# Optimization experiments

Hardware: AMD Instinct MI355X
Metric: run time of the kernel (lower is better)

Reference implementation:

```python
import jax, jax.numpy as jnp
import numpy as np

B, S, D, H, DK = 2, 2048, 256, 8, 32


def setup_inputs() -> dict:
    key = jax.random.key(0)
    ks = jax.random.split(key, 12)
    inp = {
        "query": jax.random.normal(ks[0], (B, S, D), jnp.float32),
        "key_": jax.random.normal(ks[1], (B, S, D), jnp.float32),
        "value": jax.random.normal(ks[2], (B, S, D), jnp.float32),
        "mask": jax.random.randint(ks[3], (B, S, S), 0, 2).astype(bool),
        "relation": jax.random.normal(ks[4], (B, S, S), jnp.float32) * 0.05,
        # learned params (Linear stores y = x @ W^T; we store W already transposed)
        "Wq": jax.random.normal(ks[5], (D, H * DK), jnp.float32) * 0.02,
        "Wk": jax.random.normal(ks[6], (D, H * DK), jnp.float32) * 0.02,
        "Wv": jax.random.normal(ks[7], (D, H * DK), jnp.float32) * 0.02,
        "Wfc": jax.random.normal(ks[8], (H * DK, D), jnp.float32) * 0.02,
        "bfc": jax.random.normal(ks[9], (D,), jnp.float32) * 0.02,
        "gamma": jnp.ones((D,), jnp.float32),
        "beta": jnp.zeros((D,), jnp.float32),
    }
    return inp


def _layernorm(x, gamma, beta, eps=1e-5):
    mu = jnp.mean(x, axis=-1, keepdims=True)
    var = jnp.var(x, axis=-1, keepdims=True)
    return (x - mu) * jax.lax.rsqrt(var + eps) * gamma + beta


def reference(query, key_, value, mask, relation, Wq, Wk, Wv, Wfc, bfc, gamma, beta):
    b, s, _ = query.shape
    def split_heads(x, W):
        return (x @ W).reshape(b, s, H, DK).transpose(0, 2, 1, 3)  # [B,H,S,DK]
    Q = split_heads(query, Wq)
    K = split_heads(key_, Wk)
    V = split_heads(value, Wv)
    # (Q K^T) @ relation / sqrt(dk)   -- relation broadcast over heads
    qk = jnp.einsum('bhqd,bhkd->bhqk', Q, K)          # [B,H,S,S]
    scores = jnp.einsum('bhqk,bkn->bhqn', qk, relation) / jnp.sqrt(jnp.float32(DK))
    scores = jnp.where(mask[:, None, :, :], jnp.float32(-1e9), scores)
    attn = jax.nn.softmax(scores, axis=-1)            # dropout in eval mode = identity
    att = jnp.einsum('bhqn,bhnd->bhqd', attn, V)      # [B,H,S,DK]
    att = att.transpose(0, 2, 1, 3).reshape(b, s, H * DK)
    out = att @ Wfc + bfc
    return _layernorm(out + query, gamma, beta), attn
```

## Files before the change

### kernel.cpp

```cpp
#include <hip/hip_runtime.h>

constexpr int Bc = 2, Sc = 2048, Dc = 256, Hc = 8, DKc = 32;
constexpr int BH = Bc * Hc;

typedef _Float16 f16x8 __attribute__((ext_vector_type(8)));
typedef _Float16 f16x4 __attribute__((ext_vector_type(4)));
typedef float    f32x4 __attribute__((ext_vector_type(4)));

__global__ __launch_bounds__(256) void prep_kernel(
    const float* __restrict__ query, const float* __restrict__ key_,
    const float* __restrict__ value, const float* __restrict__ Wq,
    const float* __restrict__ Wk, const float* __restrict__ Wv,
    const float* __restrict__ rel, const unsigned int* __restrict__ mask,
    _Float16* __restrict__ Qb, _Float16* __restrict__ Kt,
    _Float16* __restrict__ Vt, _Float16* __restrict__ relT,
    unsigned int* __restrict__ mbits)
{
    __shared__ __align__(16) char smem[16640];
    const int bx = blockIdx.x;
    const int t = threadIdx.x;
    if (bx < 1536) {
        constexpr int ROWS = 8;
        float (*xs)[Dc] = (float(*)[Dc])smem;
        const int z = bx >> 9;
        const int lb = bx & 511;
        const float* X = (z == 0) ? query : (z == 1) ? key_ : value;
        const float* W = (z == 0) ? Wq : (z == 1) ? Wk : Wv;
        _Float16* out = (z == 0) ? Qb : (z == 1) ? Kt : Vt;
        const int vtrans = (z != 0);
        const float scale = (z == 0) ? 0.17677669529663689f : 1.0f;
        const int r0 = lb * ROWS;
        #pragma unroll
        for (int i = 0; i < ROWS; ++i)
            xs[i][t] = X[(long)(r0 + i) * Dc + t];
        __syncthreads();
        float acc[ROWS];
        #pragma unroll
        for (int i = 0; i < ROWS; ++i) acc[i] = 0.f;
        for (int d = 0; d < Dc; ++d) {
            float w = W[d * Dc + t];
            #pragma unroll
            for (int i = 0; i < ROWS; ++i) acc[i] = fmaf(xs[i][d], w, acc[i]);
        }
        const int h = t >> 5, dk = t & 31;
        #pragma unroll
        for (int i = 0; i < ROWS; ++i) {
            int row = r0 + i;
            int b = row >> 11, s = row & 2047;
            long idx = vtrans ? (((long)(b * Hc + h) * DKc + dk) * Sc + s)
                              : (((long)(b * Hc + h) * Sc + s) * DKc + dk);
            out[idx] = (_Float16)(acc[i] * scale);
        }
    } else if (bx < 3584) {
        float (*tile)[65] = (float(*)[65])smem;
        const int idx = bx - 1536;
        const int b = idx >> 10;
        const int rem = idx & 1023;
        const int k0 = (rem >> 5) * 64, n0 = (rem & 31) * 64;
        const int r = t >> 4;
        const int c4 = (t & 15) * 4;
        const float* src = rel + (long)b * Sc * Sc;
        #pragma unroll
        for (int i = 0; i < 4; ++i) {
            f32x4 v = *(const f32x4*)&src[(long)(k0 + i * 16 + r) * Sc + n0 + c4];
            *(f32x4*)&tile[i * 16 + r][c4] = v;
        }
        __syncthreads();
        _Float16* dst = relT + (long)b * Sc * Sc;
        #pragma unroll
        for (int i = 0; i < 4; ++i) {
            const int n = i * 16 + r;
            f16x4 o;
            #pragma unroll
            for (int e = 0; e < 4; ++e) o[e] = (_Float16)tile[c4 + e][n];
            *(f16x4*)&dst[(long)(n0 + n) * Sc + k0 + c4] = o;
        }
    } else {
        const int idx = (bx - 3584) * 256 + t;
        const uint4 a = ((const uint4*)mask)[idx * 2];
        const uint4 b = ((const uint4*)mask)[idx * 2 + 1];
        unsigned int wsv[8] = {a.x, a.y, a.z, a.w, b.x, b.y, b.z, b.w};
        unsigned int r = 0;
        #pragma unroll
        for (int j = 0; j < 8; ++j) {
            unsigned int nib = (wsv[j] | (wsv[j] >> 7) | (wsv[j] >> 14) | (wsv[j] >> 21)) & 0xFu;
            r |= nib << (4 * j);
        }
        mbits[idx] = r;
    }
}

__global__ __launch_bounds__(256) void kr_kernel(
    const _Float16* __restrict__ relT, const _Float16* __restrict__ Kt,
    _Float16* __restrict__ KRT)
{
    constexpr int LDK = 72;
    __shared__ _Float16 As[64][LDK];
    __shared__ _Float16 Bs[64][LDK];
    const int b = blockIdx.z;
    const int m0 = blockIdx.y * 64;
    const int n0 = blockIdx.x * 64;
    const _Float16* Ap = relT + (long)b * Sc * Sc;
    const _Float16* Bp = Kt + (long)b * Hc * DKc * Sc;
    const int t = threadIdx.x;
    const int lane = t & 63, wave = t >> 6;
    const int wr = wave >> 1, wc = wave & 1;
    const int c = lane & 15, g = lane >> 4;
    const int lrow = t >> 2;
    const int lcol = (t & 3) * 16;
    f32x4 acc[2][2] = {};
    for (int k0 = 0; k0 < Sc; k0 += 64) {
        *(f16x8*)&As[lrow][lcol]     = *(const f16x8*)&Ap[(long)(m0 + lrow) * Sc + k0 + lcol];
        *(f16x8*)&As[lrow][lcol + 8] = *(const f16x8*)&Ap[(long)(m0 + lrow) * Sc + k0 + lcol + 8];
        *(f16x8*)&Bs[lrow][lcol]     = *(const f16x8*)&Bp[(long)(n0 + lrow) * Sc + k0 + lcol];
        *(f16x8*)&Bs[lrow][lcol + 8] = *(const f16x8*)&Bp[(long)(n0 + lrow) * Sc + k0 + lcol + 8];
        __syncthreads();
        #pragma unroll
        for (int kk = 0; kk < 2; ++kk) {
            const int kb = kk * 32 + g * 8;
            f16x8 af[2], bf[2];
            #pragma unroll
            for (int m = 0; m < 2; ++m)
                af[m] = *(const f16x8*)&As[wr * 32 + m * 16 + c][kb];
            #pragma unroll
            for (int n = 0; n < 2; ++n)
                bf[n] = *(const f16x8*)&Bs[wc * 32 + n * 16 + c][kb];
            #pragma unroll
            for (int m = 0; m < 2; ++m)
                #pragma unroll
                for (int n = 0; n < 2; ++n)
                    acc[m][n] = __builtin_amdgcn_mfma_f32_16x16x32_f16(
                        af[m], bf[n], acc[m][n], 0, 0, 0);
        }
        __syncthreads();
    }
    _Float16* outp = KRT + (long)b * Sc * 256;
    #pragma unroll
    for (int m = 0; m < 2; ++m)
        #pragma unroll
        for (int n = 0; n < 2; ++n)
            #pragma unroll
            for (int i = 0; i < 4; ++i) {
                int row = m0 + wr * 32 + m * 16 + g * 4 + i;
                int col = n0 + wc * 32 + n * 16 + c;
                outp[(long)row * 256 + col] = (_Float16)acc[m][n][i];
            }
}

__global__ __launch_bounds__(256) void attn_pv_kernel(
    const _Float16* __restrict__ Qb,
    const _Float16* __restrict__ KRT,
    const _Float16* __restrict__ Vt,
    const unsigned int* __restrict__ mbits,
    float* __restrict__ esum_p,
    float* __restrict__ accp)
{
    constexpr int NT = 128, LDP = 136;
    __shared__ _Float16 p_lds[64][LDP];
    const int bh = blockIdx.y;
    const int ns = blockIdx.z;
    const int b = bh >> 3, h = bh & 7;
    const int q0 = blockIdx.x * 64;
    const int t = threadIdx.x, lane = t & 63, w = t >> 6;
    const int c = lane & 15, g = lane >> 4;
    const int q = q0 + w * 16 + c;
    const f16x8 qf = *(const f16x8*)&Qb[((long)bh * Sc + q) * DKc + g * 8];
    const _Float16* krt = KRT + (long)b * Sc * 256 + h * 32;
    const unsigned int* mbitrow = mbits + ((long)b * Sc + q) * (Sc / 32);
    const f32x4 zero = {};
    f32x4 acc[2] = {};
    float esum = 0.f;

    for (int nt = ns * 4; nt < ns * 4 + 4; ++nt) {
        const int n0 = nt * NT;
        f32x4 s[8];
        #pragma unroll
        for (int nf = 0; nf < 8; ++nf) {
            f16x8 kf = *(const f16x8*)&krt[(long)(n0 + nf * 16 + c) * 256 + g * 8];
            s[nf] = __builtin_amdgcn_mfma_f32_16x16x32_f16(kf, qf, zero, 0, 0, 0);
        }
        const uint4 mq = *(const uint4*)&mbitrow[nt * 4];
        const unsigned int mwv[4] = {mq.x, mq.y, mq.z, mq.w};
        #pragma unroll
        for (int nf = 0; nf < 8; ++nf) {
            const unsigned int bits = mwv[nf >> 1] >> ((nf & 1) * 16 + g * 4);
            f16x4 pv;
            #pragma unroll
            for (int i = 0; i < 4; ++i) {
                float p = ((bits >> i) & 1u) ? 0.f : __expf(s[nf][i]);
                esum += p;
                pv[i] = (_Float16)p;
            }
            *(f16x4*)&p_lds[w * 16 + c][nf * 16 + g * 4] = pv;
        }
        #pragma unroll
        for (int ks = 0; ks < 4; ++ks) {
            f16x8 af = *(const f16x8*)&p_lds[w * 16 + c][ks * 32 + g * 8];
            #pragma unroll
            for (int nb = 0; nb < 2; ++nb) {
                f16x8 vf = *(const f16x8*)&Vt[((long)bh * DKc + nb * 16 + c) * Sc + n0 + ks * 32 + g * 8];
                acc[nb] = __builtin_amdgcn_mfma_f32_16x16x32_f16(af, vf, acc[nb], 0, 0, 0);
            }
        }
    }
    esum += __shfl_xor(esum, 16);
    esum += __shfl_xor(esum, 32);
    if (lane < 16)
        esum_p[((long)ns * BH + bh) * Sc + q0 + w * 16 + lane] = esum;
    #pragma unroll
    for (int nb = 0; nb < 2; ++nb)
        #pragma unroll
        for (int i = 0; i < 4; ++i) {
            const long qrow = q0 + w * 16 + g * 4 + i;
            accp[(((long)ns * BH + bh) * Sc + qrow) * 32 + nb * 16 + c] = acc[nb][i];
        }
}

__global__ __launch_bounds__(256) void finish_kernel(
    const _Float16* __restrict__ Qb,
    const _Float16* __restrict__ KRT,
    const unsigned int* __restrict__ mbits,
    const float* __restrict__ esum_p,
    const float* __restrict__ accp,
    const float* __restrict__ Wfc, const float* __restrict__ bfc,
    const float* __restrict__ query, const float* __restrict__ gamma,
    const float* __restrict__ beta,
    float* __restrict__ attn_out,
    float* __restrict__ out_ln)
{
    __shared__ __align__(16) char smem[33792];
    const int z = blockIdx.z;
    const int t = threadIdx.x;
    const long BHS = (long)BH * Sc;
    if (z < 16) {
        constexpr int LDA = 132;
        float (*a_lds)[16][LDA] = (float(*)[16][LDA])smem;
        const int nt = blockIdx.x;
        const int q0 = blockIdx.y * 64;
        const int bh = z;
        const int b = bh >> 3, h = bh & 7;
        const int lane = t & 63, w = t >> 6;
        const int c = lane & 15, g = lane >> 4;
        const int q = q0 + w * 16 + c;
        const int n0 = nt * 128;
        const f16x8 qf = *(const f16x8*)&Qb[((long)bh * Sc + q) * DKc + g * 8];
        const _Float16* krt = KRT + (long)b * Sc * 256 + h * 32;
        const long row = (long)bh * Sc + q;
        const float es = esum_p[row] + esum_p[BHS + row]
                       + esum_p[2 * BHS + row] + esum_p[3 * BHS + row];
        const float rinv = 1.f / es;
        const f32x4 zero = {};

        f32x4 s[8];
        #pragma unroll
        for (int nf = 0; nf < 8; ++nf) {
            f16x8 kf = *(const f16x8*)&krt[(long)(n0 + nf * 16 + c) * 256 + g * 8];
            s[nf] = __builtin_amdgcn_mfma_f32_16x16x32_f16(kf, qf, zero, 0, 0, 0);
        }
        const uint4 mq = *(const uint4*)&mbits[((long)b * Sc + q) * (Sc / 32) + nt * 4];
        const unsigned int mwv[4] = {mq.x, mq.y, mq.z, mq.w};
        #pragma unroll
        for (int nf = 0; nf < 8; ++nf) {
            const unsigned int bits = mwv[nf >> 1] >> ((nf & 1) * 16 + g * 4);
            f32x4 av;
            #pragma unroll
            for (int i = 0; i < 4; ++i)
                av[i] = ((bits >> i) & 1u) ? 0.f : __expf(s[nf][i]) * rinv;
            *(f32x4*)&a_lds[w][c][nf * 16 + g * 4] = av;
        }
        float* aoutw = attn_out + (long)bh * Sc * Sc
                     + (long)(q0 + w * 16 + (lane >> 5)) * Sc + (lane & 31) * 4 + n0;
        #pragma unroll
        for (int r2 = 0; r2 < 8; ++r2) {
            f32x4 v = *(const f32x4*)&a_lds[w][r2 * 2 + (lane >> 5)][(lane & 31) * 4];
            __builtin_nontemporal_store(v, (f32x4*)&aoutw[(long)(r2 * 2) * Sc]);
        }
    } else {
        float (*xs)[Dc] = (float(*)[Dc])smem;
        float (*ys)[Dc] = (float(*)[Dc])(smem + 8 * Dc * 4);
        const int flat = blockIdx.x * 32 + blockIdx.y;
        const int r0 = flat * 8;
        const int h = t >> 5, dk = t & 31;
        #pragma unroll
        for (int i = 0; i < 8; ++i) {
            const long row = r0 + i;
            const int b = (int)(row >> 11);
            const int q = (int)(row & 2047);
            const long bhq = ((long)(b * Hc + h)) * Sc + q;
            float es = 0.f, av = 0.f;
            #pragma unroll
            for (int ns = 0; ns < 4; ++ns) {
                es += esum_p[ns * BHS + bhq];
                av += accp[(ns * BHS + bhq) * 32 + dk];
            }
            xs[i][t] = av / es;
        }
        __syncthreads();
        float acc[8];
        #pragma unroll
        for (int i = 0; i < 8; ++i) acc[i] = 0.f;
        for (int d = 0; d < Dc; ++d) {
            float wv = Wfc[d * Dc + t];
            #pragma unroll
            for (int i = 0; i < 8; ++i) acc[i] = fmaf(xs[i][d], wv, acc[i]);
        }
        const float bias = bfc[t];
        #pragma unroll
        for (int i = 0; i < 8; ++i)
            ys[i][t] = acc[i] + bias + query[(long)(r0 + i) * Dc + t];
        __syncthreads();
        const int w = t >> 6, lane = t & 63;
        #pragma unroll
        for (int rr2 = 0; rr2 < 2; ++rr2) {
            const int ri = w * 2 + rr2;
            float x0 = ys[ri][lane], x1 = ys[ri][lane + 64];
            float x2 = ys[ri][lane + 128], x3 = ys[ri][lane + 192];
            float sum = x0 + x1 + x2 + x3;
            float sq = x0 * x0 + x1 * x1 + x2 * x2 + x3 * x3;
            for (int off = 32; off; off >>= 1) {
                sum += __shfl_down(sum, off);
                sq  += __shfl_down(sq, off);
            }
            sum = __shfl(sum, 0);
            sq  = __shfl(sq, 0);
            const float mu = sum * (1.f / 256.f);
            const float var = sq * (1.f / 256.f) - mu * mu;
            const float rstd = rsqrtf(var + 1e-5f);
            float* orow = out_ln + (long)(r0 + ri) * Dc;
            orow[lane]       = (x0 - mu) * rstd * gamma[lane]       + beta[lane];
            orow[lane + 64]  = (x1 - mu) * rstd * gamma[lane + 64]  + beta[lane + 64];
            orow[lane + 128] = (x2 - mu) * rstd * gamma[lane + 128] + beta[lane + 128];
            orow[lane + 192] = (x3 - mu) * rstd * gamma[lane + 192] + beta[lane + 192];
        }
    }
}

extern "C" void kernel_launch(void* const* d_in, const int* in_sizes, int n_in,
                              void* d_out, int out_size, void* d_ws, size_t ws_size,
                              hipStream_t stream)
{
    const float* query   = (const float*)d_in[0];
    const float* key_    = (const float*)d_in[1];
    const float* value   = (const float*)d_in[2];
    const unsigned int* mask = (const unsigned int*)d_in[3];
    const float* relation = (const float*)d_in[4];
    const float* Wq  = (const float*)d_in[5];
    const float* Wk  = (const float*)d_in[6];
    const float* Wv  = (const float*)d_in[7];
    const float* Wfc = (const float*)d_in[8];
    const float* bfc = (const float*)d_in[9];
    const float* gamma = (const float*)d_in[10];
    const float* beta  = (const float*)d_in[11];

    float* out_ln   = (float*)d_out;
    float* out_attn = (float*)d_out + (size_t)Bc * Sc * Dc;

    char* ws = (char*)d_ws;
    _Float16* Qb   = (_Float16*)(ws + 0);
    _Float16* Kt   = (_Float16*)(ws + 2097152);
    _Float16* Vt   = (_Float16*)(ws + 4194304);
    _Float16* relT = (_Float16*)(ws + 6291456);
    _Float16* KRT  = (_Float16*)(ws + 23068672);
    unsigned int* mbits = (unsigned int*)(ws + 25165824);
    float*    esum_p= (float*)  (ws + 26214400);
    float*    accp  = (float*)  (ws + 26738688);

    prep_kernel<<<dim3(4608), 256, 0, stream>>>(
        query, key_, value, Wq, Wk, Wv, relation, mask,
        Qb, Kt, Vt, relT, mbits);
    kr_kernel<<<dim3(4, Sc / 64, Bc), 256, 0, stream>>>(relT, Kt, KRT);
    attn_pv_kernel<<<dim3(Sc / 64, BH, 4), 256, 0, stream>>>(
        Qb, KRT, Vt, mbits, esum_p, accp);
    finish_kernel<<<dim3(Sc / 128, Sc / 64, 17), 256, 0, stream>>>(
        Qb, KRT, mbits, esum_p, accp, Wfc, bfc, query, gamma, beta,
        out_attn, out_ln);
}
```

Measured before the change: 206.9 us.

## Split finish kernel into attention-store and output/layernorm kernels with new tiling

Splits the combined finish kernel, which branched on blockIdx.z, into two kernels: one that recomputes and writes the normalized attention matrix and one that does the output projection plus layernorm. The attention kernel now gives each block 16 query rows, and each of its four waves sweeps 512 columns in four 128-column steps. The Q fragment, softmax denominator and mask row pointer are loaded once per wave and reused across the steps. The cost is an extra kernel launch, and the out-projection work no longer runs concurrently inside the same grid as the attention stores.

After: 210.5 us. Within noise of the previous version (+1.7%).

```diff
diff --git a/kernel.cpp b/kernel.cpp
--- a/kernel.cpp
+++ b/kernel.cpp
@@ -216,48 +216,43 @@
         }
 }
 
-__global__ __launch_bounds__(256) void finish_kernel(
+__global__ __launch_bounds__(256) void attn_store_kernel(
     const _Float16* __restrict__ Qb,
     const _Float16* __restrict__ KRT,
     const unsigned int* __restrict__ mbits,
     const float* __restrict__ esum_p,
-    const float* __restrict__ accp,
-    const float* __restrict__ Wfc, const float* __restrict__ bfc,
-    const float* __restrict__ query, const float* __restrict__ gamma,
-    const float* __restrict__ beta,
-    float* __restrict__ attn_out,
-    float* __restrict__ out_ln)
-{
-    __shared__ __align__(16) char smem[33792];
-    const int z = blockIdx.z;
-    const int t = threadIdx.x;
+    float* __restrict__ attn_out)
+{
+    constexpr int LDA = 132;
+    __shared__ float a_lds[4][16][LDA];
+    const int q0 = blockIdx.x * 16;
+    const int bh = blockIdx.y;
+    const int b = bh >> 3, h = bh & 7;
+    const int t = threadIdx.x, lane = t & 63, w = t >> 6;
+    const int c = lane & 15, g = lane >> 4;
+    const int q = q0 + c;
+    const f16x8 qf = *(const f16x8*)&Qb[((long)bh * Sc + q) * DKc + g * 8];
+    const _Float16* krt = KRT + (long)b * Sc * 256 + h * 32;
+    const unsigned int* mbitrow = mbits + ((long)b * Sc + q) * (Sc / 32);
+    const long row = (long)bh * Sc + q;
     const long BHS = (long)BH * Sc;
-    if (z < 16) {
-        constexpr int LDA = 132;
-        float (*a_lds)[16][LDA] = (float(*)[16][LDA])smem;
-        const int nt = blockIdx.x;
-        const int q0 = blockIdx.y * 64;
-        const int bh = z;
-        const int b = bh >> 3, h = bh & 7;
-        const int lane = t & 63, w = t >> 6;
-        const int c = lane & 15, g = lane >> 4;
-        const int q = q0 + w * 16 + c;
-        const int n0 = nt * 128;
-        const f16x8 qf = *(const f16x8*)&Qb[((long)bh * Sc + q) * DKc + g * 8];
-        const _Float16* krt = KRT + (long)b * Sc * 256 + h * 32;
-        const long row = (long)bh * Sc + q;
-        const float es = esum_p[row] + esum_p[BHS + row]
-                       + esum_p[2 * BHS + row] + esum_p[3 * BHS + row];
-        const float rinv = 1.f / es;
-        const f32x4 zero = {};
-
+    const float es = esum_p[row] + esum_p[BHS + row]
+                   + esum_p[2 * BHS + row] + esum_p[3 * BHS + row];
+    const float rinv = 1.f / es;
+    const f32x4 zero = {};
+    float* aoutw = attn_out + (long)bh * Sc * Sc
+                 + (long)(q0 + (lane >> 5)) * Sc + (lane & 31) * 4 + w * 512;
+
+    #pragma unroll
+    for (int tt = 0; tt < 4; ++tt) {
+        const int n0 = w * 512 + tt * 128;
         f32x4 s[8];
         #pragma unroll
         for (int nf = 0; nf < 8; ++nf) {
             f16x8 kf = *(const f16x8*)&krt[(long)(n0 + nf * 16 + c) * 256 + g * 8];
             s[nf] = __builtin_amdgcn_mfma_f32_16x16x32_f16(kf, qf, zero, 0, 0, 0);
         }
-        const uint4 mq = *(const uint4*)&mbits[((long)b * Sc + q) * (Sc / 32) + nt * 4];
+        const uint4 mq = *(const uint4*)&mbitrow[n0 / 32];
         const unsigned int mwv[4] = {mq.x, mq.y, mq.z, mq.w};
         #pragma unroll
         for (int nf = 0; nf < 8; ++nf) {
@@ -268,70 +263,77 @@
                 av[i] = ((bits >> i) & 1u) ? 0.f : __expf(s[nf][i]) * rinv;
             *(f32x4*)&a_lds[w][c][nf * 16 + g * 4] = av;
         }
-        float* aoutw = attn_out + (long)bh * Sc * Sc
-                     + (long)(q0 + w * 16 + (lane >> 5)) * Sc + (lane & 31) * 4 + n0;
         #pragma unroll
         for (int r2 = 0; r2 < 8; ++r2) {
             f32x4 v = *(const f32x4*)&a_lds[w][r2 * 2 + (lane >> 5)][(lane & 31) * 4];
-            __builtin_nontemporal_store(v, (f32x4*)&aoutw[(long)(r2 * 2) * Sc]);
-        }
-    } else {
-        float (*xs)[Dc] = (float(*)[Dc])smem;
-        float (*ys)[Dc] = (float(*)[Dc])(smem + 8 * Dc * 4);
-        const int flat = blockIdx.x * 32 + blockIdx.y;
-        const int r0 = flat * 8;
-        const int h = t >> 5, dk = t & 31;
-        #pragma unroll
-        for (int i = 0; i < 8; ++i) {
-            const long row = r0 + i;
-            const int b = (int)(row >> 11);
-            const int q = (int)(row & 2047);
-            const long bhq = ((long)(b * Hc + h)) * Sc + q;
-            float es = 0.f, av = 0.f;
-            #pragma unroll
-            for (int ns = 0; ns < 4; ++ns) {
-                es += esum_p[ns * BHS + bhq];
-                av += accp[(ns * BHS + bhq) * 32 + dk];
-            }
-            xs[i][t] = av / es;
-        }
-        __syncthreads();
-        float acc[8];
-        #pragma unroll
-        for (int i = 0; i < 8; ++i) acc[i] = 0.f;
-        for (int d = 0; d < Dc; ++d) {
-            float wv = Wfc[d * Dc + t];
-            #pragma unroll
-            for (int i = 0; i < 8; ++i) acc[i] = fmaf(xs[i][d], wv, acc[i]);
-        }
-        const float bias = bfc[t];
-        #pragma unroll
-        for (int i = 0; i < 8; ++i)
-            ys[i][t] = acc[i] + bias + query[(long)(r0 + i) * Dc + t];
-        __syncthreads();
-        const int w = t >> 6, lane = t & 63;
-        #pragma unroll
-        for (int rr2 = 0; rr2 < 2; ++rr2) {
-            const int ri = w * 2 + rr2;
-            float x0 = ys[ri][lane], x1 = ys[ri][lane + 64];
-            float x2 = ys[ri][lane + 128], x3 = ys[ri][lane + 192];
-            float sum = x0 + x1 + x2 + x3;
-            float sq = x0 * x0 + x1 * x1 + x2 * x2 + x3 * x3;
-            for (int off = 32; off; off >>= 1) {
-                sum += __shfl_down(sum, off);
-                sq  += __shfl_down(sq, off);
-            }
-            sum = __shfl(sum, 0);
-            sq  = __shfl(sq, 0);
-            const float mu = sum * (1.f / 256.f);
-            const float var = sq * (1.f / 256.f) - mu * mu;
-            const float rstd = rsqrtf(var + 1e-5f);
-            float* orow = out_ln + (long)(r0 + ri) * Dc;
-            orow[lane]       = (x0 - mu) * rstd * gamma[lane]       + beta[lane];
-            orow[lane + 64]  = (x1 - mu) * rstd * gamma[lane + 64]  + beta[lane + 64];
-            orow[lane + 128] = (x2 - mu) * rstd * gamma[lane + 128] + beta[lane + 128];
-            orow[lane + 192] = (x3 - mu) * rstd * gamma[lane + 192] + beta[lane + 192];
-        }
+            __builtin_nontemporal_store(v, (f32x4*)&aoutw[(long)(r2 * 2) * Sc + tt * 128]);
+        }
+    }
+}
+
+__global__ __launch_bounds__(256) void out_kernel(
+    const float* __restrict__ accp,
+    const float* __restrict__ esum_p,
+    const float* __restrict__ Wfc, const float* __restrict__ bfc,
+    const float* __restrict__ query, const float* __restrict__ gamma,
+    const float* __restrict__ beta, float* __restrict__ out)
+{
+    __shared__ float xs[8][Dc];
+    __shared__ float ys[8][Dc];
+    const int r0 = blockIdx.x * 8;
+    const int t = threadIdx.x;
+    const int h = t >> 5, dk = t & 31;
+    const long BHS = (long)BH * Sc;
+    #pragma unroll
+    for (int i = 0; i < 8; ++i) {
+        const long row = r0 + i;
+        const int b = (int)(row >> 11);
+        const int q = (int)(row & 2047);
+        const long bhq = ((long)(b * Hc + h)) * Sc + q;
+        float es = 0.f, av = 0.f;
+        #pragma unroll
+        for (int ns = 0; ns < 4; ++ns) {
+            es += esum_p[ns * BHS + bhq];
+            av += accp[(ns * BHS + bhq) * 32 + dk];
+        }
+        xs[i][t] = av / es;
+    }
+    __syncthreads();
+    float acc[8];
+    #pragma unroll
+    for (int i = 0; i < 8; ++i) acc[i] = 0.f;
+    for (int d = 0; d < Dc; ++d) {
+        float wv = Wfc[d * Dc + t];
+        #pragma unroll
+        for (int i = 0; i < 8; ++i) acc[i] = fmaf(xs[i][d], wv, acc[i]);
+    }
+    const float bias = bfc[t];
+    #pragma unroll
+    for (int i = 0; i < 8; ++i)
+        ys[i][t] = acc[i] + bias + query[(long)(r0 + i) * Dc + t];
+    __syncthreads();
+    const int w = t >> 6, lane = t & 63;
+    #pragma unroll
+    for (int rr2 = 0; rr2 < 2; ++rr2) {
+        const int ri = w * 2 + rr2;
+        float x0 = ys[ri][lane], x1 = ys[ri][lane + 64];
+        float x2 = ys[ri][lane + 128], x3 = ys[ri][lane + 192];
+        float sum = x0 + x1 + x2 + x3;
+        float sq = x0 * x0 + x1 * x1 + x2 * x2 + x3 * x3;
+        for (int off = 32; off; off >>= 1) {
+            sum += __shfl_down(sum, off);
+            sq  += __shfl_down(sq, off);
+        }
+        sum = __shfl(sum, 0);
+        sq  = __shfl(sq, 0);
+        const float mu = sum * (1.f / 256.f);
+        const float var = sq * (1.f / 256.f) - mu * mu;
+        const float rstd = rsqrtf(var + 1e-5f);
+        float* orow = out + (long)(r0 + ri) * Dc;
+        orow[lane]       = (x0 - mu) * rstd * gamma[lane]       + beta[lane];
+        orow[lane + 64]  = (x1 - mu) * rstd * gamma[lane + 64]  + beta[lane + 64];
+        orow[lane + 128] = (x2 - mu) * rstd * gamma[lane + 128] + beta[lane + 128];
+        orow[lane + 192] = (x3 - mu) * rstd * gamma[lane + 192] + beta[lane + 192];
     }
 }
 
@@ -371,7 +373,8 @@
     kr_kernel<<<dim3(4, Sc / 64, Bc), 256, 0, stream>>>(relT, Kt, KRT);
     attn_pv_kernel<<<dim3(Sc / 64, BH, 4), 256, 0, stream>>>(
         Qb, KRT, Vt, mbits, esum_p, accp);
-    finish_kernel<<<dim3(Sc / 128, Sc / 64, 17), 256, 0, stream>>>(
-        Qb, KRT, mbits, esum_p, accp, Wfc, bfc, query, gamma, beta,
-        out_attn, out_ln);
-}
+    attn_store_kernel<<<dim3(Sc / 16, BH), 256, 0, stream>>>(
+        Qb, KRT, mbits, esum_p, out_attn);
+    out_kernel<<<dim3(Bc * Sc / 8), 256, 0, stream>>>(
+        accp, esum_p, Wfc, bfc, query, gamma, beta, out_ln);
+}
```
